# Kernel tuning notes

Hardware: AMD Instinct MI355X
Metric: run time of the kernel (lower is better)

## Reference

```python
import jax, jax.numpy as jnp
import numpy as np

B, H, W, C = 32, 56, 56, 128
HEAD, WS, SHIFT = 4, 7, 3
N = WS * WS            # tokens per window = 49
NW = (H // WS) * (W // WS)  # windows per image = 64
HD = C // HEAD
SCALE = HD ** (-0.5)
HID = 4 * C


def _rel_pos_index():
    coords = np.stack(np.meshgrid(np.arange(WS), np.arange(WS), indexing='ij')).reshape(2, -1)
    rel = (coords[:, :, None] - coords[:, None, :]).transpose(1, 2, 0).copy()
    rel[:, :, 0] += WS - 1
    rel[:, :, 1] += WS - 1
    rel[:, :, 0] *= 2 * WS - 1
    return rel.sum(-1)  # (N, N) int


def _attn_mask():
    img = np.zeros((H, W))
    slices = (slice(0, -WS), slice(-WS, -SHIFT), slice(-SHIFT, None))
    cnt = 0
    for hs in slices:
        for ws_ in slices:
            img[hs, ws_] = cnt
            cnt += 1
    mw = img.reshape(H // WS, WS, W // WS, WS).transpose(0, 2, 1, 3).reshape(-1, N)
    diff = mw[:, None, :] - mw[:, :, None]  # matches unsqueeze(1) - unsqueeze(2)
    return np.where(diff != 0, -100.0, 0.0).astype(np.float32)  # (NW, N, N)

REL_IDX = jnp.asarray(_rel_pos_index())
ATTN_MASK = jnp.asarray(_attn_mask())


def setup_inputs() -> dict:
    key = jax.random.key(0)
    ks = jax.random.split(key, 8)
    s = 0.02
    return {
        'x': jax.random.normal(ks[0], (B, H * W, C), jnp.float32),
        'norm1_g': jnp.ones((C,), jnp.float32),
        'norm1_b': jnp.zeros((C,), jnp.float32),
        'qkv_w': jax.random.normal(ks[1], (C, 3 * C), jnp.float32) * s,
        'qkv_b': jnp.zeros((3 * C,), jnp.float32),
        'proj_w': jax.random.normal(ks[2], (C, C), jnp.float32) * s,
        'proj_b': jnp.zeros((C,), jnp.float32),
        'rpb_table': jax.random.normal(ks[3], ((2 * WS - 1) ** 2, HEAD), jnp.float32) * s,
        'norm2_g': jnp.ones((C,), jnp.float32),
        'norm2_b': jnp.zeros((C,), jnp.float32),
        'fc1_w': jax.random.normal(ks[4], (C, HID), jnp.float32) * s,
        'fc1_b': jnp.zeros((HID,), jnp.float32),
        'fc2_w': jax.random.normal(ks[5], (HID, C), jnp.float32) * s,
        'fc2_b': jnp.zeros((C,), jnp.float32),
    }


def _ln(x, g, b):
    m = x.mean(-1, keepdims=True)
    v = ((x - m) ** 2).mean(-1, keepdims=True)
    return (x - m) / jnp.sqrt(v + 1e-5) * g + b


def reference(x, norm1_g, norm1_b, qkv_w, qkv_b, proj_w, proj_b, rpb_table,
              norm2_g, norm2_b, fc1_w, fc1_b, fc2_w, fc2_b):
    shortcut = x
    h = _ln(x, norm1_g, norm1_b).reshape(B, H, W, C)
    # cyclic shift
    h = jnp.roll(h, shift=(-SHIFT, -SHIFT), axis=(1, 2))
    # window partition -> (B*NW, N, C)
    hw = h.reshape(B, H // WS, WS, W // WS, WS, C).transpose(0, 1, 3, 2, 4, 5).reshape(-1, N, C)
    Bw = hw.shape[0]
    # windowed attention
    qkv = (hw @ qkv_w + qkv_b).reshape(Bw, N, 3, HEAD, HD).transpose(2, 0, 3, 1, 4)
    q, k, v = qkv[0] * SCALE, qkv[1], qkv[2]
    attn = jnp.einsum('bhnd,bhmd->bhnm', q, k)
    bias = rpb_table[REL_IDX.reshape(-1)].reshape(N, N, HEAD).transpose(2, 0, 1)  # (HEAD, N, N)
    attn = attn + bias[None]
    attn = attn.reshape(B, NW, HEAD, N, N) + ATTN_MASK[None, :, None]
    attn = jax.nn.softmax(attn.reshape(Bw, HEAD, N, N), axis=-1)
    o = jnp.einsum('bhnm,bhmd->bhnd', attn, v).transpose(0, 2, 1, 3).reshape(Bw, N, C)
    o = o @ proj_w + proj_b
    # merge windows
    o = o.reshape(B, H // WS, W // WS, WS, WS, C).transpose(0, 1, 3, 2, 4, 5).reshape(B, H, W, C)
    # reverse shift
    o = jnp.roll(o, shift=(SHIFT, SHIFT), axis=(1, 2)).reshape(B, H * W, C)
    x = shortcut + o
    # MLP block
    m = _ln(x, norm2_g, norm2_b)
    m = jax.nn.gelu(m @ fc1_w + fc1_b, approximate=False) @ fc2_w + fc2_b
    return x + m
```

## Files before the change

### kernel.cpp

```cpp
#include <hip/hip_runtime.h>
#include <hip/hip_bf16.h>
#include <math.h>

#define Bb 32
#define Hh 56
#define Ww 56
#define Cc 128
#define HEAD 4
#define WS 7
#define SHIFT 3
#define Nn 49
#define NWw 64
#define HD 32
#define HID 512
#define TOK (Bb*Hh*Ww)
#define SCALEF 0.17677669529663687f
#define WSTRIDE 136
#define W2STRIDE 68

typedef short short8 __attribute__((ext_vector_type(8)));
typedef float f32x4 __attribute__((ext_vector_type(4)));

__device__ __forceinline__ short f2bf(float f) {
    union { float f; unsigned u; } c; c.f = f;
    unsigned r = (c.u + 0x7fff + ((c.u >> 16) & 1)) >> 16;
    return (short)r;
}
__device__ __forceinline__ unsigned pack2bf(float a, float b) {
    return (unsigned)(unsigned short)f2bf(a) | ((unsigned)(unsigned short)f2bf(b) << 16);
}
__device__ __forceinline__ float gelu_fast(float x) {
    float x3 = x * x * x;
    float y = 0.7978845608f * (x + 0.044715f * x3);
    float e = __expf(2.f * y);
    float t = 1.f - 2.f / (e + 1.f);
    return 0.5f * x * (1.f + t);
}
#define LDS_FENCE() asm volatile("s_waitcnt lgkmcnt(0)" ::: "memory")

__global__ void conv_t(const float* __restrict__ in, short* __restrict__ out,
                       int K, int N) {
    int idx = blockIdx.x * 256 + threadIdx.x;
    if (idx >= K * N) return;
    int k = idx / N, n = idx % N;
    out[(size_t)n * K + k] = f2bf(in[idx]);
}

__global__ void build_table(const float* __restrict__ rpb, float* __restrict__ table) {
    int idx = blockIdx.x * 256 + threadIdx.x;
    if (idx >= 16 * 4096) return;
    int cell = idx & 4095, ch = idx >> 12;
    int cls = ch >> 2, hd = ch & 3;
    int row = cell >> 6, col = cell & 63;
    float v;
    if (row >= Nn || col >= Nn) v = -1e30f;
    else {
        int i1 = row / 7, j1 = row % 7, i2 = col / 7, j2 = col % 7;
        float bias = rpb[((i1 - i2 + 6) * 13 + (j1 - j2 + 6)) * HEAD + hd];
        int bh = cls >> 1, bw = cls & 1;
        int rn = bh ? (i1 < 4 ? 1 : 2) : 0;
        int cn = bw ? (j1 < 4 ? 1 : 2) : 0;
        int rm = bh ? (i2 < 4 ? 1 : 2) : 0;
        int cm = bw ? (j2 < 4 ? 1 : 2) : 0;
        v = bias + (((rn * 3 + cn) != (rm * 3 + cm)) ? -100.f : 0.f);
    }
    table[idx] = v;
}

__global__ __launch_bounds__(256) void ln1_gather(const float* __restrict__ x,
                                                  const float* __restrict__ g,
                                                  const float* __restrict__ b,
                                                  short* __restrict__ h) {
    int wave = threadIdx.x >> 6, lane = threadIdx.x & 63;
    int t = blockIdx.x * 4 + wave;
    int bimg = t / (NWw * Nn);
    int wrow = t % (NWw * Nn);
    int wi = wrow / Nn, n = wrow % Nn;
    int wh = wi >> 3, ww = wi & 7;
    int i = n / 7, j = n % 7;
    int sr = (wh * 7 + i + SHIFT) % Hh;
    int scol = (ww * 7 + j + SHIFT) % Ww;
    const float* xr = x + ((size_t)bimg * (Hh * Ww) + sr * Ww + scol) * Cc;
    float2 v = ((const float2*)xr)[lane];
    float s = v.x + v.y;
    #pragma unroll
    for (int m = 32; m; m >>= 1) s += __shfl_xor(s, m, 64);
    float mean = s * (1.f / 128.f);
    float dx = v.x - mean, dy = v.y - mean;
    float vs = dx * dx + dy * dy;
    #pragma unroll
    for (int m = 32; m; m >>= 1) vs += __shfl_xor(vs, m, 64);
    float inv = rsqrtf(vs * (1.f / 128.f) + 1e-5f);
    float2 gg = ((const float2*)g)[lane];
    float2 bb = ((const float2*)b)[lane];
    ((unsigned*)(h + (size_t)t * Cc))[lane] =
        pack2bf(dx * inv * gg.x + bb.x, dy * inv * gg.y + bb.y);
}

__global__ __launch_bounds__(256, 3) void qkv_mfma(const short* __restrict__ h,
                                                   const short* __restrict__ wt,
                                                   const float* __restrict__ bias,
                                                   short* __restrict__ qkv) {
    __shared__ short Wc[128 * WSTRIDE];
    int tid = threadIdx.x;
    int wave = tid >> 6, lane = tid & 63;
    int row16 = lane & 15, quad = lane >> 4;
    size_t t0 = (size_t)blockIdx.x * 64 + wave * 16;
    short8 afr[4];
    #pragma unroll
    for (int k = 0; k < 4; ++k)
        afr[k] = *(const short8*)(h + (t0 + row16) * Cc + k * 32 + quad * 8);
    int srow = tid >> 4, skof = (tid & 15) * 8;
    for (int ch = 0; ch < 3; ++ch) {
        __syncthreads();
        #pragma unroll
        for (int i = 0; i < 8; ++i) {
            int r = srow + i * 16;
            short8 w = *(const short8*)(wt + (size_t)(ch * 128 + r) * Cc + skof);
            *(short8*)(Wc + r * WSTRIDE + skof) = w;
        }
        __syncthreads();
        f32x4 acc[8];
        #pragma unroll
        for (int n = 0; n < 8; ++n) acc[n] = (f32x4)(0.f);
        #pragma unroll
        for (int k = 0; k < 4; ++k) {
            #pragma unroll
            for (int n = 0; n < 8; ++n) {
                short8 bfr = *(const short8*)(Wc + (n * 16 + row16) * WSTRIDE + k * 32 + quad * 8);
                acc[n] = __builtin_amdgcn_mfma_f32_16x16x32_bf16(afr[k], bfr, acc[n], 0, 0, 0);
            }
        }
        #pragma unroll
        for (int n = 0; n < 8; ++n) {
            int col = ch * 128 + n * 16 + row16;
            float bv = bias[col];
            #pragma unroll
            for (int r = 0; r < 4; ++r) {
                float val = acc[n][r] + bv;
                if (ch == 0) val *= SCALEF;
                qkv[(t0 + quad * 4 + r) * 384 + col] = f2bf(val);
            }
        }
    }
}

__global__ __launch_bounds__(128, 3) void attn_mfma(const short* __restrict__ qkv,
                                                    const float* __restrict__ table,
                                                    short* __restrict__ o) {
    __shared__ short Pbuf[2][64 * 72];
    __shared__ short Vbuf[2][32 * 72];
    int wave = threadIdx.x >> 6, lane = threadIdx.x & 63;
    int row16 = lane & 15, quad = lane >> 4;
    int unit = blockIdx.x * 2 + wave;
    int bw = unit >> 2, hd = unit & 3;
    int widx = bw & 63, wh = widx >> 3, ww = widx & 7;
    int cls = ((wh == 7) ? 2 : 0) | ((ww == 7) ? 1 : 0);
    const float* tb = table + ((size_t)(cls * 4 + hd)) * 4096;
    short* P = &Pbuf[wave][0];
    short* vt = &Vbuf[wave][0];
    const short* base = qkv + (size_t)bw * Nn * 384 + hd * HD;

    {
        int t = lane;
        if (t < Nn) {
            const short* vrow = base + (size_t)t * 384 + 256;
            #pragma unroll
            for (int d = 0; d < HD; d += 2) {
                unsigned pr = *(const unsigned*)(vrow + d);
                vt[d * 72 + t] = (short)(pr & 0xffff);
                vt[(d + 1) * 72 + t] = (short)(pr >> 16);
            }
        } else {
            #pragma unroll
            for (int d = 0; d < HD; ++d) vt[d * 72 + t] = 0;
        }
    }

    short8 qa[4], kb[4];
    #pragma unroll
    for (int mt = 0; mt < 4; ++mt) {
        int r = mt * 16 + row16;
        if (r < Nn) {
            qa[mt] = *(const short8*)(base + (size_t)r * 384 + quad * 8);
            kb[mt] = *(const short8*)(base + (size_t)r * 384 + 128 + quad * 8);
        } else {
            qa[mt] = (short8)(short)0;
            kb[mt] = (short8)(short)0;
        }
    }
    f32x4 s[4][4];
    #pragma unroll
    for (int mt = 0; mt < 4; ++mt)
        #pragma unroll
        for (int nt = 0; nt < 4; ++nt)
            s[mt][nt] = __builtin_amdgcn_mfma_f32_16x16x32_bf16(qa[mt], kb[nt], (f32x4)(0.f), 0, 0, 0);

    #pragma unroll
    for (int mt = 0; mt < 4; ++mt) {
        #pragma unroll
        for (int r = 0; r < 4; ++r) {
            int row = mt * 16 + quad * 4 + r;
            float mx = -1e30f;
            #pragma unroll
            for (int nt = 0; nt < 4; ++nt) {
                s[mt][nt][r] += tb[row * 64 + nt * 16 + row16];
                mx = fmaxf(mx, s[mt][nt][r]);
            }
            #pragma unroll
            for (int m = 1; m < 16; m <<= 1) mx = fmaxf(mx, __shfl_xor(mx, m, 64));
            float sm = 0.f;
            #pragma unroll
            for (int nt = 0; nt < 4; ++nt) {
                float e = __expf(s[mt][nt][r] - mx);
                s[mt][nt][r] = e;
                sm += e;
            }
            #pragma unroll
            for (int m = 1; m < 16; m <<= 1) sm += __shfl_xor(sm, m, 64);
            float inv = 1.f / sm;
            #pragma unroll
            for (int nt = 0; nt < 4; ++nt)
                P[row * 72 + nt * 16 + row16] = f2bf(s[mt][nt][r] * inv);
        }
    }
    LDS_FENCE();

    f32x4 oacc[4][2];
    #pragma unroll
    for (int mt = 0; mt < 4; ++mt)
        #pragma unroll
        for (int nt = 0; nt < 2; ++nt) oacc[mt][nt] = (f32x4)(0.f);
    #pragma unroll
    for (int kt = 0; kt < 2; ++kt) {
        short8 pa[4], vb[2];
        #pragma unroll
        for (int mt = 0; mt < 4; ++mt)
            pa[mt] = *(const short8*)(P + (mt * 16 + row16) * 72 + kt * 32 + quad * 8);
        #pragma unroll
        for (int nt = 0; nt < 2; ++nt)
            vb[nt] = *(const short8*)(vt + (nt * 16 + row16) * 72 + kt * 32 + quad * 8);
        #pragma unroll
        for (int mt = 0; mt < 4; ++mt)
            #pragma unroll
            for (int nt = 0; nt < 2; ++nt)
                oacc[mt][nt] = __builtin_amdgcn_mfma_f32_16x16x32_bf16(pa[mt], vb[nt], oacc[mt][nt], 0, 0, 0);
    }
    #pragma unroll
    for (int mt = 0; mt < 4; ++mt)
        #pragma unroll
        for (int nt = 0; nt < 2; ++nt)
            #pragma unroll
            for (int r = 0; r < 4; ++r) {
                int row = mt * 16 + quad * 4 + r;
                if (row < Nn)
                    o[((size_t)bw * Nn + row) * Cc + hd * HD + nt * 16 + row16] = f2bf(oacc[mt][nt][r]);
            }
}

__global__ __launch_bounds__(256, 3) void proj_ln2(const short* __restrict__ o,
                                                   const short* __restrict__ wt,
                                                   const float* __restrict__ pb,
                                                   const float* __restrict__ x,
                                                   const float* __restrict__ g2,
                                                   const float* __restrict__ b2,
                                                   float* __restrict__ x1,
                                                   short* __restrict__ m) {
    __shared__ short Wc[128 * WSTRIDE];
    __shared__ int dest[64];
    int tid = threadIdx.x;
    int wave = tid >> 6, lane = tid & 63;
    int row16 = lane & 15, quad = lane >> 4;
    int s0 = blockIdx.x * 64;
    {
        int srow = tid >> 4, skof = (tid & 15) * 8;
        #pragma unroll
        for (int i = 0; i < 8; ++i) {
            int r = srow + i * 16;
            short8 w = *(const short8*)(wt + (size_t)r * Cc + skof);
            *(short8*)(Wc + r * WSTRIDE + skof) = w;
        }
    }
    if (tid < 64) {
        int st = s0 + tid;
        int bimg = st / (NWw * Nn);
        int rem = st % (NWw * Nn);
        int wi = rem / Nn, n = rem % Nn;
        int wh = wi >> 3, ww = wi & 7;
        int i = n / 7, j = n % 7;
        int dr = (wh * 7 + i + SHIFT) % Hh;
        int dc = (ww * 7 + j + SHIFT) % Ww;
        dest[tid] = bimg * (Hh * Ww) + dr * Ww + dc;
    }
    __syncthreads();
    int r0w = wave * 16;
    short8 afr[4];
    #pragma unroll
    for (int k = 0; k < 4; ++k)
        afr[k] = *(const short8*)(o + ((size_t)s0 + r0w + row16) * Cc + k * 32 + quad * 8);
    f32x4 acc[8];
    #pragma unroll
    for (int n = 0; n < 8; ++n) acc[n] = (f32x4)(0.f);
    #pragma unroll
    for (int k = 0; k < 4; ++k) {
        #pragma unroll
        for (int n = 0; n < 8; ++n) {
            short8 bfr = *(const short8*)(Wc + (n * 16 + row16) * WSTRIDE + k * 32 + quad * 8);
            acc[n] = __builtin_amdgcn_mfma_f32_16x16x32_bf16(afr[k], bfr, acc[n], 0, 0, 0);
        }
    }
    float gv[8], bv[8], pbv[8];
    #pragma unroll
    for (int n = 0; n < 8; ++n) {
        int col = n * 16 + row16;
        gv[n] = g2[col]; bv[n] = b2[col]; pbv[n] = pb[col];
    }
    #pragma unroll
    for (int r = 0; r < 4; ++r) {
        int di = dest[r0w + quad * 4 + r];
        #pragma unroll
        for (int n = 0; n < 8; ++n)
            acc[n][r] += x[(size_t)di * Cc + n * 16 + row16] + pbv[n];
        float sum = 0.f;
        #pragma unroll
        for (int n = 0; n < 8; ++n) sum += acc[n][r];
        #pragma unroll
        for (int mk = 1; mk < 16; mk <<= 1) sum += __shfl_xor(sum, mk, 64);
        float mean = sum * (1.f / 128.f);
        float var = 0.f;
        #pragma unroll
        for (int n = 0; n < 8; ++n) {
            float d = acc[n][r] - mean;
            var += d * d;
        }
        #pragma unroll
        for (int mk = 1; mk < 16; mk <<= 1) var += __shfl_xor(var, mk, 64);
        float inv = rsqrtf(var * (1.f / 128.f) + 1e-5f);
        #pragma unroll
        for (int n = 0; n < 8; ++n) {
            size_t idx = (size_t)di * Cc + n * 16 + row16;
            float v = acc[n][r];
            x1[idx] = v;
            m[idx] = f2bf((v - mean) * inv * gv[n] + bv[n]);
        }
    }
}

#define HSTRIDE 72
__global__ __launch_bounds__(256, 3) void mlp_mfma(const short* __restrict__ m,
                                                   const short* __restrict__ w1t,
                                                   const float* __restrict__ b1,
                                                   const short* __restrict__ w2t,
                                                   const float* __restrict__ b2,
                                                   const float* __restrict__ x1,
                                                   float* __restrict__ out) {
    __shared__ short W1c[64 * WSTRIDE];
    __shared__ short W2c[128 * W2STRIDE];
    __shared__ short Hs[4][16 * HSTRIDE];
    int tid = threadIdx.x;
    int wave = tid >> 6, lane = tid & 63;
    int row16 = lane & 15, quad = lane >> 4;
    size_t t0 = (size_t)blockIdx.x * 64 + wave * 16;
    short* Ht = &Hs[wave][0];
    short8 bfr[4];
    #pragma unroll
    for (int k = 0; k < 4; ++k)
        bfr[k] = *(const short8*)(m + (t0 + row16) * Cc + k * 32 + quad * 8);
    f32x4 acc2[8];
    #pragma unroll
    for (int n = 0; n < 8; ++n) acc2[n] = (f32x4)(0.f);

    int rA = tid >> 4, cA = (tid & 15) * 8;
    int rB = tid >> 3, cB = (tid & 7) * 8;
    short8 w1r[4], w2r[4];
    #pragma unroll
    for (int i = 0; i < 4; ++i) {
        w1r[i] = *(const short8*)(w1t + (size_t)(rA + i * 16) * Cc + cA);
        w2r[i] = *(const short8*)(w2t + (size_t)(rB + i * 32) * HID + cB);
    }

    for (int ch = 0; ch < 8; ++ch) {
        __syncthreads();
        #pragma unroll
        for (int i = 0; i < 4; ++i) {
            *(short8*)(W1c + (rA + i * 16) * WSTRIDE + cA) = w1r[i];
            *(short8*)(W2c + (rB + i * 32) * W2STRIDE + cB) = w2r[i];
        }
        if (ch < 7) {
            #pragma unroll
            for (int i = 0; i < 4; ++i) {
                w1r[i] = *(const short8*)(w1t + (size_t)((ch + 1) * 64 + rA + i * 16) * Cc + cA);
                w2r[i] = *(const short8*)(w2t + (size_t)(rB + i * 32) * HID + (ch + 1) * 64 + cB);
            }
        }
        __syncthreads();
        f32x4 acc1[4];
        #pragma unroll
        for (int mt = 0; mt < 4; ++mt) acc1[mt] = (f32x4)(0.f);
        #pragma unroll
        for (int k = 0; k < 4; ++k) {
            #pragma unroll
            for (int mt = 0; mt < 4; ++mt) {
                short8 a = *(const short8*)(W1c + (mt * 16 + row16) * WSTRIDE + k * 32 + quad * 8);
                acc1[mt] = __builtin_amdgcn_mfma_f32_16x16x32_bf16(a, bfr[k], acc1[mt], 0, 0, 0);
            }
        }
        #pragma unroll
        for (int mt = 0; mt < 4; ++mt) {
            int hidb = ch * 64 + mt * 16 + quad * 4;
            f32x4 b1v = *(const f32x4*)(b1 + hidb);
            float h0 = gelu_fast(acc1[mt][0] + b1v[0]);
            float h1 = gelu_fast(acc1[mt][1] + b1v[1]);
            float h2 = gelu_fast(acc1[mt][2] + b1v[2]);
            float h3 = gelu_fast(acc1[mt][3] + b1v[3]);
            uint2 pk;
            pk.x = pack2bf(h0, h1);
            pk.y = pack2bf(h2, h3);
            *(uint2*)(Ht + row16 * HSTRIDE + mt * 16 + quad * 4) = pk;
        }
        LDS_FENCE();
        #pragma unroll
        for (int kk = 0; kk < 2; ++kk) {
            short8 ha = *(const short8*)(Ht + row16 * HSTRIDE + kk * 32 + quad * 8);
            #pragma unroll
            for (int n = 0; n < 8; ++n) {
                short8 wb = *(const short8*)(W2c + (n * 16 + row16) * W2STRIDE + kk * 32 + quad * 8);
                acc2[n] = __builtin_amdgcn_mfma_f32_16x16x32_bf16(ha, wb, acc2[n], 0, 0, 0);
            }
        }
        LDS_FENCE();
    }
    #pragma unroll
    for (int n = 0; n < 8; ++n) {
        int col = n * 16 + row16;
        float bb = b2[col];
        #pragma unroll
        for (int r = 0; r < 4; ++r) {
            size_t idx = (t0 + quad * 4 + r) * Cc + col;
            out[idx] = x1[idx] + bb + acc2[n][r];
        }
    }
}

extern "C" void kernel_launch(void* const* d_in, const int* in_sizes, int n_in,
                              void* d_out, int out_size, void* d_ws, size_t ws_size,
                              hipStream_t stream) {
    const float* x     = (const float*)d_in[0];
    const float* n1g   = (const float*)d_in[1];
    const float* n1b   = (const float*)d_in[2];
    const float* qkvw  = (const float*)d_in[3];
    const float* qkvb  = (const float*)d_in[4];
    const float* projw = (const float*)d_in[5];
    const float* projb = (const float*)d_in[6];
    const float* rpb   = (const float*)d_in[7];
    const float* n2g   = (const float*)d_in[8];
    const float* n2b   = (const float*)d_in[9];
    const float* fc1w  = (const float*)d_in[10];
    const float* fc1b  = (const float*)d_in[11];
    const float* fc2w  = (const float*)d_in[12];
    const float* fc2b  = (const float*)d_in[13];
    float* out = (float*)d_out;

    char* ws = (char*)d_ws;
    short* qkv   = (short*)ws;
    float* x1    = (float*)(ws + 77070336);
    float* table = x1;
    short* h     = (short*)(ws + 77070336 + 51380224);
    short* m     = h;
    short* o     = (short*)(ws + 77070336 + 51380224 + 25690112);
    short* qkvwT = (short*)(ws + 77070336 + 51380224 + 2 * 25690112);
    short* projwT= qkvwT + 384 * 128;
    short* fc1wT = projwT + 128 * 128;
    short* fc2wT = fc1wT + 512 * 128;

    conv_t<<<(128 * 384 + 255) / 256, 256, 0, stream>>>(qkvw, qkvwT, 128, 384);
    conv_t<<<(128 * 128 + 255) / 256, 256, 0, stream>>>(projw, projwT, 128, 128);
    conv_t<<<(128 * 512 + 255) / 256, 256, 0, stream>>>(fc1w, fc1wT, 128, 512);
    conv_t<<<(512 * 128 + 255) / 256, 256, 0, stream>>>(fc2w, fc2wT, 512, 128);
    build_table<<<256, 256, 0, stream>>>(rpb, table);

    ln1_gather<<<TOK / 4, 256, 0, stream>>>(x, n1g, n1b, h);
    qkv_mfma<<<TOK / 64, 256, 0, stream>>>(h, qkvwT, qkvb, qkv);
    attn_mfma<<<(TOK / Nn) * HEAD / 2, 128, 0, stream>>>(qkv, table, o);
    proj_ln2<<<TOK / 64, 256, 0, stream>>>(o, projwT, projb, x, n2g, n2b, x1, m);
    mlp_mfma<<<TOK / 64, 256, 0, stream>>>(m, fc1wT, fc1b, fc2wT, fc2b, x1, out);
}
```

Baseline: 305.9 us.

## Prefetch QKV weight chunks into registers, simplify GELU, use hardware bf16 pack

The QKV kernel now loads the next weight chunk from global memory into registers while the current chunk is being multiplied, so the global load latency overlaps with compute. The tanh-based GELU is rewritten in the algebraically equivalent sigmoid form, x/(1+exp(-2y)), using a fast reciprocal, which cuts the arithmetic per element. The MLP hidden activations are packed to bf16 with the v_cvt_pk_bf16_f32 instruction instead of manual rounding code. The register prefetch raises register pressure under launch_bounds(256,3), and rcpf slightly lowers precision.

Result: faster. 294.3 us (-3.8%).

```diff
diff --git a/kernel.cpp b/kernel.cpp
--- a/kernel.cpp
+++ b/kernel.cpp
@@ -30,11 +30,15 @@
     return (unsigned)(unsigned short)f2bf(a) | ((unsigned)(unsigned short)f2bf(b) << 16);
 }
 __device__ __forceinline__ float gelu_fast(float x) {
-    float x3 = x * x * x;
-    float y = 0.7978845608f * (x + 0.044715f * x3);
-    float e = __expf(2.f * y);
-    float t = 1.f - 2.f / (e + 1.f);
-    return 0.5f * x * (1.f + t);
+    float p = x * x;
+    float v = x * (-1.5957691216f - 0.07135481627f * p);
+    float e = __expf(v);
+    return x * __builtin_amdgcn_rcpf(1.f + e);
+}
+__device__ __forceinline__ unsigned cvtpk2bf(float a, float b) {
+    unsigned r;
+    asm("v_cvt_pk_bf16_f32 %0, %1, %2" : "=v"(r) : "v"(a), "v"(b));
+    return r;
 }
 #define LDS_FENCE() asm volatile("s_waitcnt lgkmcnt(0)" ::: "memory")
 
@@ -111,13 +115,19 @@
     for (int k = 0; k < 4; ++k)
         afr[k] = *(const short8*)(h + (t0 + row16) * Cc + k * 32 + quad * 8);
     int srow = tid >> 4, skof = (tid & 15) * 8;
+    short8 wr[8];
+    #pragma unroll
+    for (int i = 0; i < 8; ++i)
+        wr[i] = *(const short8*)(wt + (size_t)(srow + i * 16) * Cc + skof);
     for (int ch = 0; ch < 3; ++ch) {
         __syncthreads();
         #pragma unroll
-        for (int i = 0; i < 8; ++i) {
-            int r = srow + i * 16;
-            short8 w = *(const short8*)(wt + (size_t)(ch * 128 + r) * Cc + skof);
-            *(short8*)(Wc + r * WSTRIDE + skof) = w;
+        for (int i = 0; i < 8; ++i)
+            *(short8*)(Wc + (srow + i * 16) * WSTRIDE + skof) = wr[i];
+        if (ch < 2) {
+            #pragma unroll
+            for (int i = 0; i < 8; ++i)
+                wr[i] = *(const short8*)(wt + (size_t)((ch + 1) * 128 + srow + i * 16) * Cc + skof);
         }
         __syncthreads();
         f32x4 acc[8];
@@ -414,8 +424,8 @@
             float h2 = gelu_fast(acc1[mt][2] + b1v[2]);
             float h3 = gelu_fast(acc1[mt][3] + b1v[3]);
             uint2 pk;
-            pk.x = pack2bf(h0, h1);
-            pk.y = pack2bf(h2, h3);
+            pk.x = cvtpk2bf(h0, h1);
+            pk.y = cvtpk2bf(h2, h3);
             *(uint2*)(Ht + row16 * HSTRIDE + mt * 16 + quad * 4) = pk;
         }
         LDS_FENCE();
```
